# Kernel tuning notes

Hardware: AMD Instinct MI355X
Metric: run time of the kernel (lower is better)

Reference implementation:

```python
import jax, jax.numpy as jnp
import numpy as np

N = 100000
E = 1600000
F_IN = 128
DIM = 32
NUM_CLASSES = 40
BN_EPS = 1e-5


def setup_inputs() -> dict:
    key = jax.random.key(0)
    ks = jax.random.split(key, 16)
    inp = {}
    inp['x'] = jax.random.normal(ks[0], (N, F_IN), dtype=jnp.float32)
    inp['edge_index'] = jax.random.randint(ks[1], (2, E), 0, N, dtype=jnp.int64)
    s = lambda fan_in: 1.0 / np.sqrt(fan_in)
    # GINConv 1 MLP: Linear(F_IN, DIM) -> ReLU -> Linear(DIM, DIM)
    inp['w1a'] = jax.random.uniform(ks[2], (F_IN, DIM), jnp.float32, -s(F_IN), s(F_IN))
    inp['b1a'] = jnp.zeros((DIM,), jnp.float32)
    inp['w1b'] = jax.random.uniform(ks[3], (DIM, DIM), jnp.float32, -s(DIM), s(DIM))
    inp['b1b'] = jnp.zeros((DIM,), jnp.float32)
    # GINConv 2 MLP: Linear(DIM, DIM) -> ReLU -> Linear(DIM, DIM)
    inp['w2a'] = jax.random.uniform(ks[4], (DIM, DIM), jnp.float32, -s(DIM), s(DIM))
    inp['b2a'] = jnp.zeros((DIM,), jnp.float32)
    inp['w2b'] = jax.random.uniform(ks[5], (DIM, DIM), jnp.float32, -s(DIM), s(DIM))
    inp['b2b'] = jnp.zeros((DIM,), jnp.float32)
    # BatchNorm params (eval mode: running stats)
    inp['bn1_g'] = jnp.ones((DIM,), jnp.float32)
    inp['bn1_b'] = jnp.zeros((DIM,), jnp.float32)
    inp['bn1_m'] = jax.random.normal(ks[6], (DIM,), jnp.float32) * 0.1
    inp['bn1_v'] = jax.random.uniform(ks[7], (DIM,), jnp.float32, 0.5, 1.5)
    inp['bn2_g'] = jnp.ones((DIM,), jnp.float32)
    inp['bn2_b'] = jnp.zeros((DIM,), jnp.float32)
    inp['bn2_m'] = jax.random.normal(ks[8], (DIM,), jnp.float32) * 0.1
    inp['bn2_v'] = jax.random.uniform(ks[9], (DIM,), jnp.float32, 0.5, 1.5)
    # FC heads
    inp['fc1_w'] = jax.random.uniform(ks[10], (DIM, DIM), jnp.float32, -s(DIM), s(DIM))
    inp['fc1_b'] = jnp.zeros((DIM,), jnp.float32)
    inp['fc2_w'] = jax.random.uniform(ks[11], (DIM, NUM_CLASSES), jnp.float32, -s(DIM), s(DIM))
    inp['fc2_b'] = jnp.zeros((NUM_CLASSES,), jnp.float32)
    return inp


def _gin_conv(x, src, dst, wa, ba, wb, bb):
    # sum-aggregate neighbor features (messages flow src -> dst), eps = 0
    agg = jax.ops.segment_sum(x[src], dst, num_segments=N)
    h = agg + x  # (1 + eps) * x + sum_j x_j
    h = jax.nn.relu(h @ wa + ba)
    return h @ wb + bb


def _bn(x, g, b, m, v):
    return (x - m) * (g * jax.lax.rsqrt(v + BN_EPS)) + b


def reference(x, edge_index, w1a, b1a, w1b, b1b, w2a, b2a, w2b, b2b,
              bn1_g, bn1_b, bn1_m, bn1_v, bn2_g, bn2_b, bn2_m, bn2_v,
              fc1_w, fc1_b, fc2_w, fc2_b):
    src, dst = edge_index[0], edge_index[1]
    h = jax.nn.relu(_gin_conv(x, src, dst, w1a, b1a, w1b, b1b))
    h = _bn(h, bn1_g, bn1_b, bn1_m, bn1_v)  # dropout is identity in eval
    h = _gin_conv(h, src, dst, w2a, b2a, w2b, b2b)
    h = _bn(h, bn2_g, bn2_b, bn2_m, bn2_v)
    h = jax.nn.relu(h @ fc1_w + fc1_b)
    logits = h @ fc2_w + fc2_b
    return jax.nn.log_softmax(logits, axis=1)
```

## Files before the change

kernel.cpp:

```cpp
#include <hip/hip_runtime.h>
#include <hip/hip_bf16.h>

static constexpr int N_   = 100000;
static constexpr int E_   = 1600000;
static constexpr int FIN_ = 128;
static constexpr int DIM_ = 32;
static constexpr int NC_  = 40;
static constexpr int NB_BKT = (N_ + 127) / 128;
static constexpr int NCHUNK = 256;
static constexpr int EPC    = E_ / NCHUNK;
static constexpr int PROJ_NB = N_ / 32;
static constexpr int CS_NB  = (NB_BKT + 7) / 8;

__device__ __forceinline__ int edge_at(const void* e, int is64, long long i) {
    return is64 ? (int)((const long long*)e)[i] : ((const int*)e)[i];
}

__device__ __forceinline__ float bflo(unsigned u) { return __uint_as_float(u << 16); }
__device__ __forceinline__ float bfhi(unsigned u) { return __uint_as_float(u & 0xffff0000u); }

#define DETECT_FLAG(edge, sflag)                                        \
    if (threadIdx.x < 64) {                                             \
        const long long* p_ = (const long long*)(edge);                 \
        long long v_ = p_[threadIdx.x];                                 \
        bool bad_ = (v_ < 0 || v_ >= (long long)N_);                    \
        unsigned long long m_ = __ballot(bad_);                         \
        if (threadIdx.x == 0) sflag = (m_ == 0ull) ? 1 : 0;             \
    }                                                                   \
    __syncthreads();

__global__ __launch_bounds__(256) void chist_kernel(const void* __restrict__ edge,
                                                    int* __restrict__ ghist) {
    __shared__ int lh[NB_BKT];
    __shared__ int sflag;
    DETECT_FLAG(edge, sflag)
    for (int i = threadIdx.x; i < NB_BKT; i += 256) lh[i] = 0;
    __syncthreads();
    int f = sflag;
    int b = blockIdx.x;
    int end = b * EPC + EPC;
    for (int e = b * EPC + threadIdx.x; e < end; e += 256) {
        int d = edge_at(edge, f, (long long)E_ + e);
        atomicAdd(&lh[d >> 7], 1);
    }
    __syncthreads();
    for (int i = threadIdx.x; i < NB_BKT; i += 256) ghist[b * NB_BKT + i] = lh[i];
}

__global__ __launch_bounds__(256) void colscan_kernel(const int* __restrict__ ghist,
                                                      int* __restrict__ gcur,
                                                      int* __restrict__ bcnt,
                                                      int* __restrict__ bbase,
                                                      int* __restrict__ offs,
                                                      int* __restrict__ done) {
    __shared__ int tile[256 * 9];
    __shared__ int a[256];
    __shared__ int lastFlag;
    int tid = threadIdx.x;
    int k0 = blockIdx.x * 8;

    {
        int kk = tid & 7, r0 = tid >> 3;
        for (int p = 0; p < 8; ++p) {
            int b = r0 + p * 32;
            int k = k0 + kk;
            tile[b * 9 + kk] = (k < NB_BKT) ? ghist[b * NB_BKT + k] : 0;
        }
    }
    __syncthreads();

    int c = tid >> 5, lane = tid & 31;
    int v[8]; int s = 0;
#pragma unroll
    for (int r = 0; r < 8; ++r) { v[r] = tile[(lane * 8 + r) * 9 + c]; s += v[r]; }
    int incl = s;
#pragma unroll
    for (int off = 1; off < 32; off <<= 1) {
        int u = __shfl_up(incl, off, 32);
        if (lane >= off) incl += u;
    }
    int ex = incl - s;
    int k = k0 + c;
    if (k < NB_BKT) {
        int run = ex;
#pragma unroll
        for (int r = 0; r < 8; ++r) {
            int b = lane * 8 + r;
            gcur[b * NB_BKT + k] = run;
            run += v[r];
        }
        if (lane == 31) bcnt[k] = run;
    }
    __syncthreads();
    if (tid == 0) {
        __threadfence();
        int old = atomicAdd(done, 1);
        lastFlag = (old == CS_NB - 1) ? 1 : 0;
    }
    __syncthreads();
    if (lastFlag) {
        __threadfence();
        int b4[4]; int base4 = tid * 4; int t = 0;
#pragma unroll
        for (int j = 0; j < 4; ++j) { int i = base4 + j; b4[j] = (i < NB_BKT) ? bcnt[i] : 0; t += b4[j]; }
        a[tid] = t;
        __syncthreads();
        for (int off = 1; off < 256; off <<= 1) {
            int u = a[tid] + ((tid >= off) ? a[tid - off] : 0);
            __syncthreads(); a[tid] = u; __syncthreads();
        }
        int g = a[tid] - t;
#pragma unroll
        for (int j = 0; j < 4; ++j) { int i = base4 + j; if (i < NB_BKT) bbase[i] = g; g += b4[j]; }
        if (tid == 255) offs[N_] = a[255];
    }
}

__global__ __launch_bounds__(256) void dscatter_kernel(const void* __restrict__ edge,
                                                       const int* __restrict__ bbase,
                                                       const int* __restrict__ gcur,
                                                       int* __restrict__ packed) {
    __shared__ int cur[NB_BKT];
    __shared__ int sflag;
    DETECT_FLAG(edge, sflag)
    int b = blockIdx.x, tid = threadIdx.x;
    for (int k = tid; k < NB_BKT; k += 256) cur[k] = bbase[k] + gcur[b * NB_BKT + k];
    __syncthreads();
    int f = sflag;
    int end = b * EPC + EPC;
    for (int e = b * EPC + tid; e < end; e += 256) {
        int s = edge_at(edge, f, e);
        int d = edge_at(edge, f, (long long)E_ + e);
        int pos = atomicAdd(&cur[d >> 7], 1);
        packed[pos] = s | ((d & 127) << 17);
    }
}

__global__ __launch_bounds__(256) void fat_kernel(const int* __restrict__ bcnt,
                                                  const int* __restrict__ bbase,
                                                  const int* __restrict__ packed,
                                                  int* __restrict__ offs,
                                                  int* __restrict__ csr,
                                                  const float* __restrict__ x,
                                                  const float* __restrict__ w,
                                                  __hip_bfloat16* __restrict__ yh) {
    __shared__ __align__(16) char smem[32768];
    int tid = threadIdx.x;
    if (blockIdx.x < NB_BKT) {
        int* c   = (int*)smem;
        int* cur = (int*)smem + 128;
        int b = blockIdx.x;
        int beg = bbase[b], cnt = bcnt[b];
        if (tid < 128) c[tid] = 0;
        __syncthreads();
        for (int i = tid; i < cnt; i += 256)
            atomicAdd(&c[packed[beg + i] >> 17], 1);
        __syncthreads();
        int myv = (tid < 128) ? c[tid] : 0;
        for (int off = 1; off < 128; off <<= 1) {
            int t = 0;
            if (tid < 128) t = c[tid] + ((tid >= off) ? c[tid - off] : 0);
            __syncthreads();
            if (tid < 128) c[tid] = t;
            __syncthreads();
        }
        if (tid < 128) {
            int ex = c[tid] - myv;
            cur[tid] = ex;
            int node = b * 128 + tid;
            if (node < N_) offs[node] = beg + ex;
        }
        __syncthreads();
        for (int i = tid; i < cnt; i += 256) {
            int v = packed[beg + i];
            int p = atomicAdd(&cur[v >> 17], 1);
            csr[beg + p] = v & 0x1FFFF;
        }
    } else {
        float* wsm = (float*)smem;
        float* xs  = (float*)(smem + 16384);
        const float4* w4 = (const float4*)w;
        float4* ws4 = (float4*)wsm;
        for (int i = tid; i < FIN_ * DIM_ / 4; i += 256) ws4[i] = w4[i];

        int nodeBase = (blockIdx.x - NB_BKT) * 32;
        const float4* x4 = (const float4*)(x + (size_t)nodeBase * FIN_);
        float4* xs4 = (float4*)xs;
        for (int i = tid; i < 32 * FIN_ / 4; i += 256) xs4[i] = x4[i];
        __syncthreads();

        int d = tid & 31, ns = tid >> 5;
        for (int rep = 0; rep < 4; ++rep) {
            int node = ns + rep * 8;
            float acc = 0.f;
#pragma unroll 4
            for (int k = 0; k < FIN_; ++k) acc += xs[node * FIN_ + k] * wsm[k * DIM_ + d];
            yh[(size_t)(nodeBase + node) * DIM_ + d] = __float2bfloat16(acc);
        }
    }
}

__device__ __forceinline__ void gather_row(const int* __restrict__ csr,
                                           const char* __restrict__ vb,
                                           int beg, int end, int loff,
                                           float& a0, float& a1, float& a2, float& a3) {
    int i = beg;
    for (; i + 3 < end; i += 4) {
        int s0 = csr[i], s1 = csr[i + 1], s2 = csr[i + 2], s3 = csr[i + 3];
        uint2 u0 = *(const uint2*)(vb + (((size_t)s0) << 6) + loff);
        uint2 u1 = *(const uint2*)(vb + (((size_t)s1) << 6) + loff);
        uint2 u2 = *(const uint2*)(vb + (((size_t)s2) << 6) + loff);
        uint2 u3 = *(const uint2*)(vb + (((size_t)s3) << 6) + loff);
        a0 += (bflo(u0.x) + bflo(u1.x)) + (bflo(u2.x) + bflo(u3.x));
        a1 += (bfhi(u0.x) + bfhi(u1.x)) + (bfhi(u2.x) + bfhi(u3.x));
        a2 += (bflo(u0.y) + bflo(u1.y)) + (bflo(u2.y) + bflo(u3.y));
        a3 += (bfhi(u0.y) + bfhi(u1.y)) + (bfhi(u2.y) + bfhi(u3.y));
    }
    for (; i < end; ++i) {
        int s0 = csr[i];
        uint2 u0 = *(const uint2*)(vb + (((size_t)s0) << 6) + loff);
        a0 += bflo(u0.x); a1 += bfhi(u0.x); a2 += bflo(u0.y); a3 += bfhi(u0.y);
    }
}

__global__ __launch_bounds__(256) void aggmlp1_kernel(const int* __restrict__ offs,
                                                      const int* __restrict__ csr,
                                                      const __hip_bfloat16* __restrict__ yh,
                                                      const float* __restrict__ b1a,
                                                      const float* __restrict__ w1b,
                                                      const float* __restrict__ b1b,
                                                      const float* __restrict__ g1,
                                                      const float* __restrict__ be1,
                                                      const float* __restrict__ m1,
                                                      const float* __restrict__ v1,
                                                      const float* __restrict__ w2a,
                                                      __hip_bfloat16* __restrict__ zh) {
    __shared__ float A[32 * 33];
    __shared__ float B[32 * 33];
    __shared__ float w1s[DIM_ * DIM_];
    __shared__ float w2s[DIM_ * DIM_];
    int tid = threadIdx.x;
    for (int i = tid; i < DIM_ * DIM_; i += 256) { w1s[i] = w1b[i]; w2s[i] = w2a[i]; }

    int nl = tid >> 3, lane = tid & 7;
    int node = blockIdx.x * 32 + nl;
    int beg = offs[node], end = offs[node + 1];
    float a0 = 0.f, a1 = 0.f, a2 = 0.f, a3 = 0.f;
    gather_row(csr, (const char*)yh, beg, end, lane << 3, a0, a1, a2, a3);
    {
        float* p = &A[nl * 33 + lane * 4];
        p[0] = a0; p[1] = a1; p[2] = a2; p[3] = a3;
    }
    __syncthreads();

    int d = tid & 31, ng = tid >> 5;
    size_t gbase = (size_t)blockIdx.x * 32 * DIM_;

#pragma unroll
    for (int r = 0; r < 4; ++r) {
        int n = r * 8 + ng;
        float yv = __bfloat162float(yh[gbase + n * DIM_ + d]);
        A[n * 33 + d] = fmaxf(A[n * 33 + d] + yv + b1a[d], 0.f);
    }
    __syncthreads();

    float sc1 = g1[d] * rsqrtf(v1[d] + 1e-5f);
    float sh1 = be1[d] - m1[d] * sc1;

#pragma unroll
    for (int r = 0; r < 4; ++r) {
        int n = r * 8 + ng;
        float s = b1b[d];
#pragma unroll
        for (int k = 0; k < DIM_; ++k) s += A[n * 33 + k] * w1s[k * DIM_ + d];
        B[n * 33 + d] = fmaxf(s, 0.f) * sc1 + sh1;
    }
    __syncthreads();

#pragma unroll
    for (int r = 0; r < 4; ++r) {
        int n = r * 8 + ng;
        float s = 0.f;
#pragma unroll
        for (int k = 0; k < DIM_; ++k) s += B[n * 33 + k] * w2s[k * DIM_ + d];
        zh[gbase + n * DIM_ + d] = __float2bfloat16(s);
    }
}

__global__ __launch_bounds__(256) void aggmlp2_kernel(const int* __restrict__ offs,
                                                      const int* __restrict__ csr,
                                                      const __hip_bfloat16* __restrict__ zh,
                                                      const float* __restrict__ b2a,
                                                      const float* __restrict__ w2b,
                                                      const float* __restrict__ b2b,
                                                      const float* __restrict__ g2,
                                                      const float* __restrict__ be2,
                                                      const float* __restrict__ m2,
                                                      const float* __restrict__ v2,
                                                      const float* __restrict__ f1w,
                                                      const float* __restrict__ f1b,
                                                      const float* __restrict__ f2w,
                                                      const float* __restrict__ f2b,
                                                      float* __restrict__ out) {
    __shared__ float A[32 * 33];
    __shared__ float BC[DIM_ * NC_];
    __shared__ float wA[DIM_ * DIM_];
    __shared__ float wB[DIM_ * DIM_];
    int tid = threadIdx.x;
    for (int i = tid; i < DIM_ * DIM_; i += 256) { wA[i] = w2b[i]; wB[i] = f1w[i]; }

    int nl = tid >> 3, lane = tid & 7;
    int node = blockIdx.x * 32 + nl;
    int beg = offs[node], end = offs[node + 1];
    float a0 = 0.f, a1 = 0.f, a2 = 0.f, a3 = 0.f;
    gather_row(csr, (const char*)zh, beg, end, lane << 3, a0, a1, a2, a3);
    {
        float* p = &A[nl * 33 + lane * 4];
        p[0] = a0; p[1] = a1; p[2] = a2; p[3] = a3;
    }
    __syncthreads();

    int d = tid & 31, ng = tid >> 5;
    size_t gbase = (size_t)blockIdx.x * 32 * DIM_;

#pragma unroll
    for (int r = 0; r < 4; ++r) {
        int n = r * 8 + ng;
        float zv = __bfloat162float(zh[gbase + n * DIM_ + d]);
        A[n * 33 + d] = fmaxf(A[n * 33 + d] + zv + b2a[d], 0.f);
    }
    __syncthreads();

    float sc2 = g2[d] * rsqrtf(v2[d] + 1e-5f);
    float sh2 = be2[d] - m2[d] * sc2;

#pragma unroll
    for (int r = 0; r < 4; ++r) {
        int n = r * 8 + ng;
        float s = b2b[d];
#pragma unroll
        for (int k = 0; k < DIM_; ++k) s += A[n * 33 + k] * wA[k * DIM_ + d];
        BC[n * 33 + d] = s * sc2 + sh2;
    }
    __syncthreads();

#pragma unroll
    for (int r = 0; r < 4; ++r) {
        int n = r * 8 + ng;
        float s = f1b[d];
#pragma unroll
        for (int k = 0; k < DIM_; ++k) s += BC[n * 33 + k] * wB[k * DIM_ + d];
        A[n * 33 + d] = fmaxf(s, 0.f);
    }
    __syncthreads();
    for (int i = tid; i < DIM_ * NC_; i += 256) BC[i] = f2w[i];
    __syncthreads();

    int c2 = 32 + (d & 7);
#pragma unroll
    for (int r = 0; r < 4; ++r) {
        int n = r * 8 + ng;
        float l0 = f2b[d];
        float l1 = f2b[c2];
#pragma unroll
        for (int k = 0; k < DIM_; ++k) {
            float fv = A[n * 33 + k];
            l0 += fv * BC[k * NC_ + d];
            l1 += fv * BC[k * NC_ + c2];
        }
        float mx = fmaxf(l0, l1);
#pragma unroll
        for (int off = 16; off; off >>= 1) mx = fmaxf(mx, __shfl_xor(mx, off));
        float se = __expf(l0 - mx) + ((d < 8) ? __expf(l1 - mx) : 0.f);
#pragma unroll
        for (int off = 16; off; off >>= 1) se += __shfl_xor(se, off);
        float lse = mx + __logf(se);
        size_t ob = (size_t)(blockIdx.x * 32 + n) * NC_;
        out[ob + d] = l0 - lse;
        if (d < 8) out[ob + 32 + d] = l1 - lse;
    }
}

extern "C" void kernel_launch(void* const* d_in, const int* in_sizes, int n_in,
                              void* d_out, int out_size, void* d_ws, size_t ws_size,
                              hipStream_t stream) {
    const float* x   = (const float*)d_in[0];
    const void*  edg = d_in[1];
    const float* w1a = (const float*)d_in[2];
    const float* b1a = (const float*)d_in[3];
    const float* w1b = (const float*)d_in[4];
    const float* b1b = (const float*)d_in[5];
    const float* w2a = (const float*)d_in[6];
    const float* b2a = (const float*)d_in[7];
    const float* w2b = (const float*)d_in[8];
    const float* b2b = (const float*)d_in[9];
    const float* g1  = (const float*)d_in[10];
    const float* be1 = (const float*)d_in[11];
    const float* m1  = (const float*)d_in[12];
    const float* v1  = (const float*)d_in[13];
    const float* g2  = (const float*)d_in[14];
    const float* be2 = (const float*)d_in[15];
    const float* m2  = (const float*)d_in[16];
    const float* v2  = (const float*)d_in[17];
    const float* f1w = (const float*)d_in[18];
    const float* f1b = (const float*)d_in[19];
    const float* f2w = (const float*)d_in[20];
    const float* f2b = (const float*)d_in[21];
    float* out = (float*)d_out;

    char* ws = (char*)d_ws;
    int* done   = (int*)ws;
    int* bcnt   = (int*)(ws + 256);
    int* bbase  = (int*)(ws + 3584);
    int* ghist  = (int*)(ws + 6912);
    int* gcur   = (int*)(ws + 807680);
    int* offs   = (int*)(ws + 1608448);
    int* packed = (int*)(ws + 2008576);
    int* csr    = (int*)(ws + 8408576);
    __hip_bfloat16* yh = (__hip_bfloat16*)(ws + 14808576);
    __hip_bfloat16* zh = (__hip_bfloat16*)(ws + 21208576);

    hipMemsetAsync(done, 0, 4, stream);

    chist_kernel<<<NCHUNK, 256, 0, stream>>>(edg, ghist);
    colscan_kernel<<<CS_NB, 256, 0, stream>>>(ghist, gcur, bcnt, bbase, offs, done);
    dscatter_kernel<<<NCHUNK, 256, 0, stream>>>(edg, bbase, gcur, packed);
    fat_kernel<<<NB_BKT + PROJ_NB, 256, 0, stream>>>(bcnt, bbase, packed, offs, csr,
                                                     x, w1a, yh);

    aggmlp1_kernel<<<N_ / 32, 256, 0, stream>>>(offs, csr, yh, b1a, w1b, b1b,
                                                g1, be1, m1, v1, w2a, zh);

    aggmlp2_kernel<<<N_ / 32, 256, 0, stream>>>(offs, csr, zh, b2a, w2b, b2b,
                                                g2, be2, m2, v2, f1w, f1b,
                                                f2w, f2b, out);
}
```

Baseline: 325.7 us.

## Split gather from MLP and register-tile the dense layers over 128-node blocks

Each fused gather+MLP kernel is split in two. A lightweight gather kernel writes the relu'd aggregate as fp32 to a workspace buffer. A separate MLP kernel then processes 128 nodes per block, with each thread computing a 4x4 register tile from float4 shared-memory loads. The input projection in the fat kernel gets the same 4x4 register tiling over 128-node blocks, staging x in two K halves. This aims to cut LDS traffic and scalar FMA overhead in the dense layers and to let the gather kernels run with less shared memory. The cost is an extra fp32 intermediate round-trip through global memory for each layer, plus two more kernel launches.

```diff
diff --git a/kernel.cpp b/kernel.cpp
--- a/kernel.cpp
+++ b/kernel.cpp
@@ -9,7 +9,7 @@
 static constexpr int NB_BKT = (N_ + 127) / 128;
 static constexpr int NCHUNK = 256;
 static constexpr int EPC    = E_ / NCHUNK;
-static constexpr int PROJ_NB = N_ / 32;
+static constexpr int MLP_NB = (N_ + 127) / 128;
 static constexpr int CS_NB  = (NB_BKT + 7) / 8;
 
 __device__ __forceinline__ int edge_at(const void* e, int is64, long long i) {
@@ -18,6 +18,12 @@
 
 __device__ __forceinline__ float bflo(unsigned u) { return __uint_as_float(u << 16); }
 __device__ __forceinline__ float bfhi(unsigned u) { return __uint_as_float(u & 0xffff0000u); }
+
+__device__ __forceinline__ unsigned pack2bf(float a, float b) {
+    __hip_bfloat16 ha = __float2bfloat16(a), hb = __float2bfloat16(b);
+    unsigned ua = *(const unsigned short*)&ha, ub = *(const unsigned short*)&hb;
+    return ua | (ub << 16);
+}
 
 #define DETECT_FLAG(edge, sflag)                                        \
     if (threadIdx.x < 64) {                                             \
@@ -28,6 +34,26 @@
         if (threadIdx.x == 0) sflag = (m_ == 0ull) ? 1 : 0;             \
     }                                                                   \
     __syncthreads();
+
+__device__ __forceinline__ void stage_acc(const float* __restrict__ Asm,
+                                          const float* __restrict__ Wsm,
+                                          int nq, int d0, float4 acc[4]) {
+#pragma unroll
+    for (int kc = 0; kc < 8; ++kc) {
+        float4 w0 = *(const float4*)&Wsm[(kc * 4 + 0) * 32 + d0];
+        float4 w1 = *(const float4*)&Wsm[(kc * 4 + 1) * 32 + d0];
+        float4 w2 = *(const float4*)&Wsm[(kc * 4 + 2) * 32 + d0];
+        float4 w3 = *(const float4*)&Wsm[(kc * 4 + 3) * 32 + d0];
+#pragma unroll
+        for (int i = 0; i < 4; ++i) {
+            float4 a = *(const float4*)&Asm[(nq + 32 * i) * 36 + kc * 4];
+            acc[i].x += a.x * w0.x + a.y * w1.x + a.z * w2.x + a.w * w3.x;
+            acc[i].y += a.x * w0.y + a.y * w1.y + a.z * w2.y + a.w * w3.y;
+            acc[i].z += a.x * w0.z + a.y * w1.z + a.z * w2.z + a.w * w3.z;
+            acc[i].w += a.x * w0.w + a.y * w1.w + a.z * w2.w + a.w * w3.w;
+        }
+    }
+}
 
 __global__ __launch_bounds__(256) void chist_kernel(const void* __restrict__ edge,
                                                     int* __restrict__ ghist) {
@@ -144,7 +170,7 @@
                                                   const float* __restrict__ x,
                                                   const float* __restrict__ w,
                                                   __hip_bfloat16* __restrict__ yh) {
-    __shared__ __align__(16) char smem[32768];
+    __shared__ __align__(16) char smem[51200];
     int tid = threadIdx.x;
     if (blockIdx.x < NB_BKT) {
         int* c   = (int*)smem;
@@ -183,19 +209,49 @@
         float4* ws4 = (float4*)wsm;
         for (int i = tid; i < FIN_ * DIM_ / 4; i += 256) ws4[i] = w4[i];
 
-        int nodeBase = (blockIdx.x - NB_BKT) * 32;
-        const float4* x4 = (const float4*)(x + (size_t)nodeBase * FIN_);
-        float4* xs4 = (float4*)xs;
-        for (int i = tid; i < 32 * FIN_ / 4; i += 256) xs4[i] = x4[i];
-        __syncthreads();
-
-        int d = tid & 31, ns = tid >> 5;
-        for (int rep = 0; rep < 4; ++rep) {
-            int node = ns + rep * 8;
-            float acc = 0.f;
-#pragma unroll 4
-            for (int k = 0; k < FIN_; ++k) acc += xs[node * FIN_ + k] * wsm[k * DIM_ + d];
-            yh[(size_t)(nodeBase + node) * DIM_ + d] = __float2bfloat16(acc);
+        int pb = blockIdx.x - NB_BKT;
+        int nodeBase = pb * 128;
+        int nq = tid >> 3, dq = tid & 7, d0 = dq * 4;
+        const float4* x4 = (const float4*)x;
+
+        float4 acc[4];
+#pragma unroll
+        for (int i = 0; i < 4; ++i) acc[i] = make_float4(0.f, 0.f, 0.f, 0.f);
+
+        for (int kh = 0; kh < 2; ++kh) {
+            __syncthreads();
+#pragma unroll
+            for (int p = 0; p < 8; ++p) {
+                int idx = tid + 256 * p;
+                int n = idx >> 4, c4 = idx & 15;
+                int gn = nodeBase + n; if (gn >= N_) gn = N_ - 1;
+                *(float4*)&xs[n * 68 + c4 * 4] = x4[(size_t)gn * 32 + kh * 16 + c4];
+            }
+            __syncthreads();
+#pragma unroll
+            for (int kc = 0; kc < 16; ++kc) {
+                int kg = kh * 64 + kc * 4;
+                float4 w0 = *(const float4*)&wsm[(kg + 0) * 32 + d0];
+                float4 w1 = *(const float4*)&wsm[(kg + 1) * 32 + d0];
+                float4 w2 = *(const float4*)&wsm[(kg + 2) * 32 + d0];
+                float4 w3 = *(const float4*)&wsm[(kg + 3) * 32 + d0];
+#pragma unroll
+                for (int i = 0; i < 4; ++i) {
+                    float4 a = *(const float4*)&xs[(nq + 32 * i) * 68 + kc * 4];
+                    acc[i].x += a.x * w0.x + a.y * w1.x + a.z * w2.x + a.w * w3.x;
+                    acc[i].y += a.x * w0.y + a.y * w1.y + a.z * w2.y + a.w * w3.y;
+                    acc[i].z += a.x * w0.z + a.y * w1.z + a.z * w2.z + a.w * w3.z;
+                    acc[i].w += a.x * w0.w + a.y * w1.w + a.z * w2.w + a.w * w3.w;
+                }
+            }
+        }
+#pragma unroll
+        for (int i = 0; i < 4; ++i) {
+            int gn = nodeBase + nq + 32 * i;
+            uint2 pk;
+            pk.x = pack2bf(acc[i].x, acc[i].y);
+            pk.y = pack2bf(acc[i].z, acc[i].w);
+            *(uint2*)((char*)yh + (size_t)gn * 64 + d0 * 2) = pk;
         }
     }
 }
@@ -223,161 +279,223 @@
     }
 }
 
-__global__ __launch_bounds__(256) void aggmlp1_kernel(const int* __restrict__ offs,
-                                                      const int* __restrict__ csr,
-                                                      const __hip_bfloat16* __restrict__ yh,
-                                                      const float* __restrict__ b1a,
-                                                      const float* __restrict__ w1b,
-                                                      const float* __restrict__ b1b,
-                                                      const float* __restrict__ g1,
-                                                      const float* __restrict__ be1,
-                                                      const float* __restrict__ m1,
-                                                      const float* __restrict__ v1,
-                                                      const float* __restrict__ w2a,
-                                                      __hip_bfloat16* __restrict__ zh) {
-    __shared__ float A[32 * 33];
-    __shared__ float B[32 * 33];
+__global__ __launch_bounds__(256) void gathu_kernel(const int* __restrict__ offs,
+                                                    const int* __restrict__ csr,
+                                                    const __hip_bfloat16* __restrict__ vh,
+                                                    const float* __restrict__ bias,
+                                                    float* __restrict__ u) {
+    int tid = threadIdx.x;
+    int nl = tid >> 3, slot = tid & 7;
+    int node = blockIdx.x * 32 + nl;
+    int beg = offs[node], end = offs[node + 1];
+    float a0 = 0.f, a1 = 0.f, a2 = 0.f, a3 = 0.f;
+    gather_row(csr, (const char*)vh, beg, end, slot << 3, a0, a1, a2, a3);
+    uint2 uy = *(const uint2*)((const char*)vh + (((size_t)node) << 6) + (slot << 3));
+    float4 bv = ((const float4*)bias)[slot];
+    float4 r;
+    r.x = fmaxf(a0 + bflo(uy.x) + bv.x, 0.f);
+    r.y = fmaxf(a1 + bfhi(uy.x) + bv.y, 0.f);
+    r.z = fmaxf(a2 + bflo(uy.y) + bv.z, 0.f);
+    r.w = fmaxf(a3 + bfhi(uy.y) + bv.w, 0.f);
+    ((float4*)u)[(size_t)blockIdx.x * 256 + tid] = r;
+}
+
+__global__ __launch_bounds__(256) void mlp1_kernel(const float* __restrict__ u,
+                                                   const float* __restrict__ w1b,
+                                                   const float* __restrict__ b1b,
+                                                   const float* __restrict__ g1,
+                                                   const float* __restrict__ be1,
+                                                   const float* __restrict__ m1,
+                                                   const float* __restrict__ v1,
+                                                   const float* __restrict__ w2a,
+                                                   __hip_bfloat16* __restrict__ zh) {
+    __shared__ __align__(16) float A[128 * 36];
+    __shared__ __align__(16) float B[128 * 36];
     __shared__ float w1s[DIM_ * DIM_];
     __shared__ float w2s[DIM_ * DIM_];
     int tid = threadIdx.x;
     for (int i = tid; i < DIM_ * DIM_; i += 256) { w1s[i] = w1b[i]; w2s[i] = w2a[i]; }
-
-    int nl = tid >> 3, lane = tid & 7;
-    int node = blockIdx.x * 32 + nl;
-    int beg = offs[node], end = offs[node + 1];
-    float a0 = 0.f, a1 = 0.f, a2 = 0.f, a3 = 0.f;
-    gather_row(csr, (const char*)yh, beg, end, lane << 3, a0, a1, a2, a3);
-    {
-        float* p = &A[nl * 33 + lane * 4];
-        p[0] = a0; p[1] = a1; p[2] = a2; p[3] = a3;
-    }
-    __syncthreads();
-
-    int d = tid & 31, ng = tid >> 5;
-    size_t gbase = (size_t)blockIdx.x * 32 * DIM_;
-
-#pragma unroll
-    for (int r = 0; r < 4; ++r) {
-        int n = r * 8 + ng;
-        float yv = __bfloat162float(yh[gbase + n * DIM_ + d]);
-        A[n * 33 + d] = fmaxf(A[n * 33 + d] + yv + b1a[d], 0.f);
-    }
-    __syncthreads();
-
-    float sc1 = g1[d] * rsqrtf(v1[d] + 1e-5f);
-    float sh1 = be1[d] - m1[d] * sc1;
-
-#pragma unroll
-    for (int r = 0; r < 4; ++r) {
-        int n = r * 8 + ng;
-        float s = b1b[d];
-#pragma unroll
-        for (int k = 0; k < DIM_; ++k) s += A[n * 33 + k] * w1s[k * DIM_ + d];
-        B[n * 33 + d] = fmaxf(s, 0.f) * sc1 + sh1;
-    }
-    __syncthreads();
-
-#pragma unroll
-    for (int r = 0; r < 4; ++r) {
-        int n = r * 8 + ng;
-        float s = 0.f;
-#pragma unroll
-        for (int k = 0; k < DIM_; ++k) s += B[n * 33 + k] * w2s[k * DIM_ + d];
-        zh[gbase + n * DIM_ + d] = __float2bfloat16(s);
-    }
-}
-
-__global__ __launch_bounds__(256) void aggmlp2_kernel(const int* __restrict__ offs,
-                                                      const int* __restrict__ csr,
-                                                      const __hip_bfloat16* __restrict__ zh,
-                                                      const float* __restrict__ b2a,
-                                                      const float* __restrict__ w2b,
-                                                      const float* __restrict__ b2b,
-                                                      const float* __restrict__ g2,
-                                                      const float* __restrict__ be2,
-                                                      const float* __restrict__ m2,
-                                                      const float* __restrict__ v2,
-                                                      const float* __restrict__ f1w,
-                                                      const float* __restrict__ f1b,
-                                                      const float* __restrict__ f2w,
-                                                      const float* __restrict__ f2b,
-                                                      float* __restrict__ out) {
-    __shared__ float A[32 * 33];
-    __shared__ float BC[DIM_ * NC_];
+    {
+        const float4* u4 = (const float4*)u + (size_t)blockIdx.x * 1024;
+#pragma unroll
+        for (int p = 0; p < 4; ++p) {
+            int idx = tid + 256 * p;
+            int n = idx >> 3, sl = idx & 7;
+            *(float4*)&A[n * 36 + sl * 4] = u4[idx];
+        }
+    }
+    __syncthreads();
+
+    int nq = tid >> 3, dq = tid & 7, d0 = dq * 4;
+
+    float4 gq = *(const float4*)&g1[d0];
+    float4 vq = *(const float4*)&v1[d0];
+    float4 bq = *(const float4*)&be1[d0];
+    float4 mq = *(const float4*)&m1[d0];
+    float4 sc, sh;
+    sc.x = gq.x * rsqrtf(vq.x + 1e-5f); sc.y = gq.y * rsqrtf(vq.y + 1e-5f);
+    sc.z = gq.z * rsqrtf(vq.z + 1e-5f); sc.w = gq.w * rsqrtf(vq.w + 1e-5f);
+    sh.x = bq.x - mq.x * sc.x; sh.y = bq.y - mq.y * sc.y;
+    sh.z = bq.z - mq.z * sc.z; sh.w = bq.w - mq.w * sc.w;
+
+    {
+        float4 bb = *(const float4*)&b1b[d0];
+        float4 acc[4];
+#pragma unroll
+        for (int i = 0; i < 4; ++i) acc[i] = bb;
+        stage_acc(A, w1s, nq, d0, acc);
+#pragma unroll
+        for (int i = 0; i < 4; ++i) {
+            float4 o;
+            o.x = fmaxf(acc[i].x, 0.f) * sc.x + sh.x;
+            o.y = fmaxf(acc[i].y, 0.f) * sc.y + sh.y;
+            o.z = fmaxf(acc[i].z, 0.f) * sc.z + sh.z;
+            o.w = fmaxf(acc[i].w, 0.f) * sc.w + sh.w;
+            *(float4*)&B[(nq + 32 * i) * 36 + d0] = o;
+        }
+    }
+    __syncthreads();
+
+    {
+        float4 acc[4];
+#pragma unroll
+        for (int i = 0; i < 4; ++i) acc[i] = make_float4(0.f, 0.f, 0.f, 0.f);
+        stage_acc(B, w2s, nq, d0, acc);
+#pragma unroll
+        for (int i = 0; i < 4; ++i) {
+            int gn = blockIdx.x * 128 + nq + 32 * i;
+            uint2 pk;
+            pk.x = pack2bf(acc[i].x, acc[i].y);
+            pk.y = pack2bf(acc[i].z, acc[i].w);
+            *(uint2*)((char*)zh + (size_t)gn * 64 + d0 * 2) = pk;
+        }
+    }
+}
+
+__global__ __launch_bounds__(256) void mlp2_kernel(const float* __restrict__ u,
+                                                   const float* __restrict__ w2b,
+                                                   const float* __restrict__ b2b,
+                                                   const float* __restrict__ g2,
+                                                   const float* __restrict__ be2,
+                                                   const float* __restrict__ m2,
+                                                   const float* __restrict__ v2,
+                                                   const float* __restrict__ f1w,
+                                                   const float* __restrict__ f1b,
+                                                   const float* __restrict__ f2w,
+                                                   const float* __restrict__ f2b,
+                                                   float* __restrict__ out) {
+    __shared__ __align__(16) float A[128 * 36];
+    __shared__ __align__(16) float B[128 * 36];
     __shared__ float wA[DIM_ * DIM_];
     __shared__ float wB[DIM_ * DIM_];
+    __shared__ float wC[DIM_ * NC_];
     int tid = threadIdx.x;
     for (int i = tid; i < DIM_ * DIM_; i += 256) { wA[i] = w2b[i]; wB[i] = f1w[i]; }
-
-    int nl = tid >> 3, lane = tid & 7;
-    int node = blockIdx.x * 32 + nl;
-    int beg = offs[node], end = offs[node + 1];
-    float a0 = 0.f, a1 = 0.f, a2 = 0.f, a3 = 0.f;
-    gather_row(csr, (const char*)zh, beg, end, lane << 3, a0, a1, a2, a3);
-    {
-        float* p = &A[nl * 33 + lane * 4];
-        p[0] = a0; p[1] = a1; p[2] = a2; p[3] = a3;
-    }
-    __syncthreads();
-
-    int d = tid & 31, ng = tid >> 5;
-    size_t gbase = (size_t)blockIdx.x * 32 * DIM_;
-
-#pragma unroll
-    for (int r = 0; r < 4; ++r) {
-        int n = r * 8 + ng;
-        float zv = __bfloat162float(zh[gbase + n * DIM_ + d]);
-        A[n * 33 + d] = fmaxf(A[n * 33 + d] + zv + b2a[d], 0.f);
-    }
-    __syncthreads();
-
-    float sc2 = g2[d] * rsqrtf(v2[d] + 1e-5f);
-    float sh2 = be2[d] - m2[d] * sc2;
-
-#pragma unroll
-    for (int r = 0; r < 4; ++r) {
-        int n = r * 8 + ng;
-        float s = b2b[d];
-#pragma unroll
-        for (int k = 0; k < DIM_; ++k) s += A[n * 33 + k] * wA[k * DIM_ + d];
-        BC[n * 33 + d] = s * sc2 + sh2;
-    }
-    __syncthreads();
-
-#pragma unroll
-    for (int r = 0; r < 4; ++r) {
-        int n = r * 8 + ng;
-        float s = f1b[d];
-#pragma unroll
-        for (int k = 0; k < DIM_; ++k) s += BC[n * 33 + k] * wB[k * DIM_ + d];
-        A[n * 33 + d] = fmaxf(s, 0.f);
-    }
-    __syncthreads();
-    for (int i = tid; i < DIM_ * NC_; i += 256) BC[i] = f2w[i];
-    __syncthreads();
-
-    int c2 = 32 + (d & 7);
-#pragma unroll
-    for (int r = 0; r < 4; ++r) {
-        int n = r * 8 + ng;
-        float l0 = f2b[d];
-        float l1 = f2b[c2];
-#pragma unroll
-        for (int k = 0; k < DIM_; ++k) {
-            float fv = A[n * 33 + k];
-            l0 += fv * BC[k * NC_ + d];
-            l1 += fv * BC[k * NC_ + c2];
-        }
-        float mx = fmaxf(l0, l1);
-#pragma unroll
-        for (int off = 16; off; off >>= 1) mx = fmaxf(mx, __shfl_xor(mx, off));
-        float se = __expf(l0 - mx) + ((d < 8) ? __expf(l1 - mx) : 0.f);
-#pragma unroll
-        for (int off = 16; off; off >>= 1) se += __shfl_xor(se, off);
-        float lse = mx + __logf(se);
-        size_t ob = (size_t)(blockIdx.x * 32 + n) * NC_;
-        out[ob + d] = l0 - lse;
-        if (d < 8) out[ob + 32 + d] = l1 - lse;
+    for (int i = tid; i < DIM_ * NC_; i += 256) wC[i] = f2w[i];
+    {
+        const float4* u4 = (const float4*)u + (size_t)blockIdx.x * 1024;
+#pragma unroll
+        for (int p = 0; p < 4; ++p) {
+            int idx = tid + 256 * p;
+            int n = idx >> 3, sl = idx & 7;
+            *(float4*)&A[n * 36 + sl * 4] = u4[idx];
+        }
+    }
+    __syncthreads();
+
+    int nq = tid >> 3, dq = tid & 7, d0 = dq * 4;
+
+    float4 gq = *(const float4*)&g2[d0];
+    float4 vq = *(const float4*)&v2[d0];
+    float4 bq = *(const float4*)&be2[d0];
+    float4 mq = *(const float4*)&m2[d0];
+    float4 sc, sh;
+    sc.x = gq.x * rsqrtf(vq.x + 1e-5f); sc.y = gq.y * rsqrtf(vq.y + 1e-5f);
+    sc.z = gq.z * rsqrtf(vq.z + 1e-5f); sc.w = gq.w * rsqrtf(vq.w + 1e-5f);
+    sh.x = bq.x - mq.x * sc.x; sh.y = bq.y - mq.y * sc.y;
+    sh.z = bq.z - mq.z * sc.z; sh.w = bq.w - mq.w * sc.w;
+
+    {
+        float4 bb = *(const float4*)&b2b[d0];
+        float4 acc[4];
+#pragma unroll
+        for (int i = 0; i < 4; ++i) acc[i] = bb;
+        stage_acc(A, wA, nq, d0, acc);
+#pragma unroll
+        for (int i = 0; i < 4; ++i) {
+            float4 o;
+            o.x = acc[i].x * sc.x + sh.x;
+            o.y = acc[i].y * sc.y + sh.y;
+            o.z = acc[i].z * sc.z + sh.z;
+            o.w = acc[i].w * sc.w + sh.w;
+            *(float4*)&B[(nq + 32 * i) * 36 + d0] = o;
+        }
+    }
+    __syncthreads();
+
+    {
+        float4 bb = *(const float4*)&f1b[d0];
+        float4 acc[4];
+#pragma unroll
+        for (int i = 0; i < 4; ++i) acc[i] = bb;
+        stage_acc(B, wB, nq, d0, acc);
+#pragma unroll
+        for (int i = 0; i < 4; ++i) {
+            float4 o;
+            o.x = fmaxf(acc[i].x, 0.f); o.y = fmaxf(acc[i].y, 0.f);
+            o.z = fmaxf(acc[i].z, 0.f); o.w = fmaxf(acc[i].w, 0.f);
+            *(float4*)&A[(nq + 32 * i) * 36 + d0] = o;
+        }
+    }
+    __syncthreads();
+
+    {
+        float4 bb = *(const float4*)&f2b[d0];
+        float be = f2b[32 + dq];
+        float4 acc[4];
+        float acce[4];
+#pragma unroll
+        for (int i = 0; i < 4; ++i) { acc[i] = bb; acce[i] = be; }
+#pragma unroll
+        for (int kc = 0; kc < 8; ++kc) {
+            float4 w0 = *(const float4*)&wC[(kc * 4 + 0) * NC_ + d0];
+            float4 w1 = *(const float4*)&wC[(kc * 4 + 1) * NC_ + d0];
+            float4 w2 = *(const float4*)&wC[(kc * 4 + 2) * NC_ + d0];
+            float4 w3 = *(const float4*)&wC[(kc * 4 + 3) * NC_ + d0];
+            float e0 = wC[(kc * 4 + 0) * NC_ + 32 + dq];
+            float e1 = wC[(kc * 4 + 1) * NC_ + 32 + dq];
+            float e2 = wC[(kc * 4 + 2) * NC_ + 32 + dq];
+            float e3 = wC[(kc * 4 + 3) * NC_ + 32 + dq];
+#pragma unroll
+            for (int i = 0; i < 4; ++i) {
+                float4 a = *(const float4*)&A[(nq + 32 * i) * 36 + kc * 4];
+                acc[i].x += a.x * w0.x + a.y * w1.x + a.z * w2.x + a.w * w3.x;
+                acc[i].y += a.x * w0.y + a.y * w1.y + a.z * w2.y + a.w * w3.y;
+                acc[i].z += a.x * w0.z + a.y * w1.z + a.z * w2.z + a.w * w3.z;
+                acc[i].w += a.x * w0.w + a.y * w1.w + a.z * w2.w + a.w * w3.w;
+                acce[i]  += a.x * e0   + a.y * e1   + a.z * e2   + a.w * e3;
+            }
+        }
+#pragma unroll
+        for (int i = 0; i < 4; ++i) {
+            float mx = fmaxf(fmaxf(fmaxf(acc[i].x, acc[i].y), fmaxf(acc[i].z, acc[i].w)), acce[i]);
+#pragma unroll
+            for (int off = 1; off < 8; off <<= 1) mx = fmaxf(mx, __shfl_xor(mx, off, 8));
+            float se = __expf(acc[i].x - mx) + __expf(acc[i].y - mx)
+                     + __expf(acc[i].z - mx) + __expf(acc[i].w - mx)
+                     + __expf(acce[i] - mx);
+#pragma unroll
+            for (int off = 1; off < 8; off <<= 1) se += __shfl_xor(se, off, 8);
+            float lse = mx + __logf(se);
+            int gn = blockIdx.x * 128 + nq + 32 * i;
+            if (gn < N_) {
+                float4 o;
+                o.x = acc[i].x - lse; o.y = acc[i].y - lse;
+                o.z = acc[i].z - lse; o.w = acc[i].w - lse;
+                *(float4*)&out[(size_t)gn * NC_ + d0] = o;
+                out[(size_t)gn * NC_ + 32 + dq] = acce[i] - lse;
+            }
+        }
     }
 }
 
@@ -415,23 +533,24 @@
     int* ghist  = (int*)(ws + 6912);
     int* gcur   = (int*)(ws + 807680);
     int* offs   = (int*)(ws + 1608448);
-    int* packed = (int*)(ws + 2008576);
-    int* csr    = (int*)(ws + 8408576);
-    __hip_bfloat16* yh = (__hip_bfloat16*)(ws + 14808576);
-    __hip_bfloat16* zh = (__hip_bfloat16*)(ws + 21208576);
+    int* packed = (int*)(ws + 2008832);
+    int* csr    = (int*)(ws + 8408832);
+    __hip_bfloat16* yh = (__hip_bfloat16*)(ws + 14808832);
+    __hip_bfloat16* zh = (__hip_bfloat16*)(ws + 21214976);
+    float* u    = (float*)(ws + 27621120);
 
     hipMemsetAsync(done, 0, 4, stream);
 
     chist_kernel<<<NCHUNK, 256, 0, stream>>>(edg, ghist);
     colscan_kernel<<<CS_NB, 256, 0, stream>>>(ghist, gcur, bcnt, bbase, offs, done);
     dscatter_kernel<<<NCHUNK, 256, 0, stream>>>(edg, bbase, gcur, packed);
-    fat_kernel<<<NB_BKT + PROJ_NB, 256, 0, stream>>>(bcnt, bbase, packed, offs, csr,
-                                                     x, w1a, yh);
-
-    aggmlp1_kernel<<<N_ / 32, 256, 0, stream>>>(offs, csr, yh, b1a, w1b, b1b,
-                                                g1, be1, m1, v1, w2a, zh);
-
-    aggmlp2_kernel<<<N_ / 32, 256, 0, stream>>>(offs, csr, zh, b2a, w2b, b2b,
-                                                g2, be2, m2, v2, f1w, f1b,
-                                                f2w, f2b, out);
-}
+    fat_kernel<<<NB_BKT + MLP_NB, 256, 0, stream>>>(bcnt, bbase, packed, offs, csr,
+                                                    x, w1a, yh);
+
+    gathu_kernel<<<N_ / 32, 256, 0, stream>>>(offs, csr, yh, b1a, u);
+    mlp1_kernel<<<MLP_NB, 256, 0, stream>>>(u, w1b, b1b, g1, be1, m1, v1, w2a, zh);
+
+    gathu_kernel<<<N_ / 32, 256, 0, stream>>>(offs, csr, zh, b2a, u);
+    mlp2_kernel<<<MLP_NB, 256, 0, stream>>>(u, w2b, b2b, g2, be2, m2, v2,
+                                            f1w, f1b, f2w, f2b, out);
+}
```

New measurement: 332.5 us. 2.1% more time.
